# Kernel tuning notes

Hardware: AMD Instinct MI355X
Metric: run time of the kernel (lower is better)

## Reference

```python
import jax, jax.numpy as jnp
import numpy as np

N_SYM = 128
BATCH = 131072
LEVERAGE = 30.0


def setup_inputs() -> dict:
    key = jax.random.key(0)
    ks = jax.random.split(key, 8)
    fractions = jax.random.normal(ks[0], (N_SYM, BATCH), dtype=jnp.float32)
    # exec_samples are Bernoulli(0/1) execution indicators, kept as float
    exec_samples = jnp.round(jax.random.uniform(ks[1], (N_SYM, BATCH), dtype=jnp.float32))
    pos_sizes = jax.random.normal(ks[2], (N_SYM, BATCH), dtype=jnp.float32)
    # margin rates strictly positive
    margin_rates = jax.random.uniform(ks[3], (N_SYM, BATCH), dtype=jnp.float32) * 0.9 + 0.1
    unused_margin = jax.random.uniform(ks[4], (BATCH,), dtype=jnp.float32) * 1000.0
    # per-symbol volume constraints: min == step (typical broker config), max >> min
    msm_step = jax.random.uniform(ks[5], (N_SYM,), dtype=jnp.float32) * 0.01 + 0.01
    msm_min = msm_step
    msm_max = msm_step * 1000.0
    return {
        "fractions": fractions,
        "exec_samples": exec_samples,
        "pos_sizes": pos_sizes,
        "margin_rates": margin_rates,
        "unused_margin": unused_margin,
        "msm_min": msm_min,
        "msm_step": msm_step,
        "msm_max": msm_max,
    }


def reference(fractions, exec_samples, pos_sizes, margin_rates, unused_margin,
              msm_min, msm_step, msm_max):
    """JAX port of LowLevelInferenceEngine._compute_new_pos_sizes.

    Sequential recurrence over traded symbols (axis 0), carrying
    unused_margin [BATCH]. Returns (new_pos_sizes [N_SYM, BATCH],
    final unused_margin [BATCH]).
    """

    def step_fn(um, xs):
        frac, ex, pos, mr, mn, st, mx = xs
        unused_size = um * mr * LEVERAGE
        max_pos_size = jnp.abs(pos) + unused_size
        # torch.where(pos*frac > 0, unused_size, max_pos_size).minimum(0)
        adj = jnp.minimum(jnp.where(pos * frac > 0, unused_size, max_pos_size), 0.0)
        new_pos_size = frac * (max_pos_size - adj)
        abs_nps = jnp.abs(new_pos_size)
        sgn = jnp.sign(new_pos_size)
        abs_nps = jnp.floor(abs_nps / st) * st
        abs_nps = jnp.where(abs_nps < mn, 0.0, abs_nps)
        abs_nps = jnp.minimum(abs_nps, mx)
        out = ex * (sgn * abs_nps) + (1.0 - ex) * pos
        um_new = (max_pos_size - abs_nps) / (mr * LEVERAGE)
        return um_new, out

    um_final, new_pos_sizes = jax.lax.scan(
        step_fn,
        unused_margin,
        (fractions, exec_samples, pos_sizes, margin_rates, msm_min, msm_step, msm_max),
    )
    return new_pos_sizes, um_final
```

## Files before the change

kernel.cpp:

```cpp
#include <hip/hip_runtime.h>
#include <math.h>

#define N_SYM 128
#define BATCH 131072
#define LEV   30.0f
#define CPB   512
#define SPP   4
#define NPH   (N_SYM / SPP)

__device__ __forceinline__ void gload16(const float* g, float* l)
{
    __builtin_amdgcn_global_load_lds(
        (const __attribute__((address_space(1))) void*)g,
        (__attribute__((address_space(3))) void*)l,
        16, 0, 0);
}

__device__ __forceinline__ float step1(float f, float e, float p, float m,
                                       float st, float mn, float mx,
                                       float* um)
{
    const float mrl = m * LEV;
    const float us  = *um * mrl;
    const float mps = fabsf(p) + us;
    const float adj = fminf((p * f > 0.0f) ? us : mps, 0.0f);
    const float nps = f * (mps - adj);

    float       a  = fabsf(nps);
    const float sg = copysignf(1.0f, nps);
    a = floorf(a / st) * st;
    a = (a < mn) ? 0.0f : a;
    a = fminf(a, mx);

    *um = (mps - a) / mrl;
    return e * (sg * a) + (1.0f - e) * p;
}

#define VMWAIT(N) asm volatile("s_waitcnt vmcnt(" #N ")" ::: "memory")
#define BARRIER() do { __builtin_amdgcn_s_barrier(); \
                       asm volatile("" ::: "memory"); } while (0)

__global__ __launch_bounds__(512) void lle_coop_kernel(
    const float* __restrict__ frac,
    const float* __restrict__ exs,
    const float* __restrict__ pos,
    const float* __restrict__ mrate,
    const float* __restrict__ um0,
    const float* __restrict__ msm_min,
    const float* __restrict__ msm_step,
    const float* __restrict__ msm_max,
    float* __restrict__ out)
{
    __shared__ float lds[4 * SPP * 4 * CPB];

    const int t     = threadIdx.x;
    const int wave  = t >> 6;
    const int lane  = t & 63;
    const int gcol0 = blockIdx.x * CPB;

    const int aidx = wave >> 1;
    const float* src = (aidx == 0) ? frac : (aidx == 1) ? exs
                     : (aidx == 2) ? pos  : mrate;
    const size_t scol = (size_t)gcol0 + (size_t)((wave & 1) * 256 + lane * 4);
    const int    wlds = aidx * 512 + (wave & 1) * 256;

    auto issue = [&](int slot) {
        const int rb = (slot & 3) * 8192 + wlds;
#pragma unroll
        for (int j = 0; j < SPP; ++j)
            gload16(src + (size_t)(slot * SPP + j) * BATCH + scol,
                    &lds[rb + j * 2048]);
    };

    float um = um0[gcol0 + t];

    auto compute = [&](int k) {
        const int rb = (k & 3) * 8192;
#pragma unroll
        for (int j = 0; j < SPP; ++j) {
            const int   s  = k * SPP + j;
            const float st = msm_step[s];
            const float mn = msm_min[s];
            const float mx = msm_max[s];
            const float f  = lds[rb + j * 2048 +        t];
            const float e  = lds[rb + j * 2048 +  512 + t];
            const float pv = lds[rb + j * 2048 + 1024 + t];
            const float m  = lds[rb + j * 2048 + 1536 + t];
            const float r  = step1(f, e, pv, m, st, mn, mx, &um);
            __builtin_nontemporal_store(r, &out[(size_t)s * BATCH + gcol0 + t]);
        }
    };

    issue(0);
    issue(1);

    issue(2);  VMWAIT(8);  BARRIER();  compute(0);
    issue(3);  VMWAIT(12); BARRIER();  compute(1);

    for (int k = 2; k <= NPH - 3; ++k) {
        issue(k + 2);
        VMWAIT(16);
        BARRIER();
        compute(k);
    }

    VMWAIT(12); BARRIER(); compute(30);
    VMWAIT(8);  BARRIER(); compute(31);

    __builtin_nontemporal_store(um, &out[(size_t)N_SYM * BATCH + gcol0 + t]);
}

extern "C" void kernel_launch(void* const* d_in, const int* in_sizes, int n_in,
                              void* d_out, int out_size, void* d_ws, size_t ws_size,
                              hipStream_t stream) {
    const float* frac     = (const float*)d_in[0];
    const float* exs      = (const float*)d_in[1];
    const float* pos      = (const float*)d_in[2];
    const float* mrate    = (const float*)d_in[3];
    const float* um0      = (const float*)d_in[4];
    const float* msm_min  = (const float*)d_in[5];
    const float* msm_step = (const float*)d_in[6];
    const float* msm_max  = (const float*)d_in[7];
    float* out = (float*)d_out;

    const int block = 512;
    const int grid  = BATCH / CPB;

    hipLaunchKernelGGL(lle_coop_kernel, dim3(grid), dim3(block), 0, stream,
                       frac, exs, pos, mrate, um0, msm_min, msm_step, msm_max,
                       out);
}
```

Baseline: 269.0 us.

## Restructure into single-wave blocks with wave-private LDS ring and vector stores

Replaces the 512-thread cooperative block, where waves loaded different arrays and synchronized with barriers, with 64-thread single-wave blocks. Each wave loads all four input arrays for its own 64 columns into a 4-deep LDS ring via global_load_lds, so no barriers are needed. Outputs are staged through LDS and written as 16-byte vector stores. The goal is to remove barrier stalls and raise the number of independent blocks in flight. In exchange there are many more blocks, a deeper per-wave prefetch with tighter vmcnt accounting, and reliance on in-wave ordering of LDS writes and reads without explicit sync.

```diff
diff --git a/kernel.cpp b/kernel.cpp
--- a/kernel.cpp
+++ b/kernel.cpp
@@ -4,9 +4,10 @@
 #define N_SYM 128
 #define BATCH 131072
 #define LEV   30.0f
-#define CPB   512
-#define SPP   4
-#define NPH   (N_SYM / SPP)
+#define RING  4
+#define NGRP  (N_SYM / 4)
+
+typedef float v4 __attribute__((ext_vector_type(4)));
 
 __device__ __forceinline__ void gload16(const float* g, float* l)
 {
@@ -37,10 +38,8 @@
 }
 
 #define VMWAIT(N) asm volatile("s_waitcnt vmcnt(" #N ")" ::: "memory")
-#define BARRIER() do { __builtin_amdgcn_s_barrier(); \
-                       asm volatile("" ::: "memory"); } while (0)
 
-__global__ __launch_bounds__(512) void lle_coop_kernel(
+__global__ __launch_bounds__(64) void lle_wave_kernel(
     const float* __restrict__ frac,
     const float* __restrict__ exs,
     const float* __restrict__ pos,
@@ -51,63 +50,63 @@
     const float* __restrict__ msm_max,
     float* __restrict__ out)
 {
-    __shared__ float lds[4 * SPP * 4 * CPB];
+    __shared__ __align__(16) float lin[RING][4][4][64];
+    __shared__ __align__(16) float lout[4][64];
 
-    const int t     = threadIdx.x;
-    const int wave  = t >> 6;
-    const int lane  = t & 63;
-    const int gcol0 = blockIdx.x * CPB;
+    const int l       = threadIdx.x;
+    const int colbase = blockIdx.x * 64;
 
-    const int aidx = wave >> 1;
-    const float* src = (aidx == 0) ? frac : (aidx == 1) ? exs
-                     : (aidx == 2) ? pos  : mrate;
-    const size_t scol = (size_t)gcol0 + (size_t)((wave & 1) * 256 + lane * 4);
-    const int    wlds = aidx * 512 + (wave & 1) * 256;
+    const float* srcs[4] = { frac, exs, pos, mrate };
 
-    auto issue = [&](int slot) {
-        const int rb = (slot & 3) * 8192 + wlds;
+    const size_t lrow = (size_t)(l >> 4);
+    const size_t lcol = (size_t)colbase + 4 * (l & 15);
+
+    auto issue = [&](int g) {
+        const int slot = g & (RING - 1);
+        const size_t row = (size_t)g * 4 + lrow;
 #pragma unroll
-        for (int j = 0; j < SPP; ++j)
-            gload16(src + (size_t)(slot * SPP + j) * BATCH + scol,
-                    &lds[rb + j * 2048]);
+        for (int A = 0; A < 4; ++A)
+            gload16(srcs[A] + row * BATCH + lcol, &lin[slot][A][0][0]);
     };
 
-    float um = um0[gcol0 + t];
+    float um = um0[colbase + l];
 
-    auto compute = [&](int k) {
-        const int rb = (k & 3) * 8192;
+    auto consume = [&](int g) {
+        const int slot = g & (RING - 1);
 #pragma unroll
-        for (int j = 0; j < SPP; ++j) {
-            const int   s  = k * SPP + j;
+        for (int j = 0; j < 4; ++j) {
+            const int   s  = g * 4 + j;
             const float st = msm_step[s];
             const float mn = msm_min[s];
             const float mx = msm_max[s];
-            const float f  = lds[rb + j * 2048 +        t];
-            const float e  = lds[rb + j * 2048 +  512 + t];
-            const float pv = lds[rb + j * 2048 + 1024 + t];
-            const float m  = lds[rb + j * 2048 + 1536 + t];
-            const float r  = step1(f, e, pv, m, st, mn, mx, &um);
-            __builtin_nontemporal_store(r, &out[(size_t)s * BATCH + gcol0 + t]);
+            const float f  = lin[slot][0][j][l];
+            const float e  = lin[slot][1][j][l];
+            const float pv = lin[slot][2][j][l];
+            const float m  = lin[slot][3][j][l];
+            lout[j][l] = step1(f, e, pv, m, st, mn, mx, &um);
         }
+        const v4 ro = *(const v4*)&lout[l >> 4][4 * (l & 15)];
+        __builtin_nontemporal_store(
+            ro, (v4*)(out + ((size_t)g * 4 + lrow) * BATCH + lcol));
     };
 
-    issue(0);
-    issue(1);
+    issue(0); issue(1); issue(2);
 
-    issue(2);  VMWAIT(8);  BARRIER();  compute(0);
-    issue(3);  VMWAIT(12); BARRIER();  compute(1);
+    issue(3); VMWAIT(12); consume(0);
+    issue(4); VMWAIT(12); consume(1);
+    issue(5); VMWAIT(12); consume(2);
 
-    for (int k = 2; k <= NPH - 3; ++k) {
-        issue(k + 2);
-        VMWAIT(16);
-        BARRIER();
-        compute(k);
+    for (int g = 3; g <= NGRP - 4; ++g) {
+        issue(g + 3);
+        VMWAIT(15);
+        consume(g);
     }
 
-    VMWAIT(12); BARRIER(); compute(30);
-    VMWAIT(8);  BARRIER(); compute(31);
+    VMWAIT(11); consume(NGRP - 3);
+    VMWAIT(7);  consume(NGRP - 2);
+    VMWAIT(3);  consume(NGRP - 1);
 
-    __builtin_nontemporal_store(um, &out[(size_t)N_SYM * BATCH + gcol0 + t]);
+    __builtin_nontemporal_store(um, &out[(size_t)N_SYM * BATCH + colbase + l]);
 }
 
 extern "C" void kernel_launch(void* const* d_in, const int* in_sizes, int n_in,
@@ -123,10 +122,10 @@
     const float* msm_max  = (const float*)d_in[7];
     float* out = (float*)d_out;
 
-    const int block = 512;
-    const int grid  = BATCH / CPB;
+    const int block = 64;
+    const int grid  = BATCH / 64;
 
-    hipLaunchKernelGGL(lle_coop_kernel, dim3(grid), dim3(block), 0, stream,
+    hipLaunchKernelGGL(lle_wave_kernel, dim3(grid), dim3(block), 0, stream,
                        frac, exs, pos, mrate, um0, msm_min, msm_step, msm_max,
                        out);
 }
```

Measured after the change: 285.1 us. 1.06x slower.
